# Kernel optimization log

Measured on AMD Instinct MI355X. Metric: run time of the kernel, lower is better.

The kernel has to match this reference:

```python
import jax, jax.numpy as jnp
import numpy as np

B = 256          # graph pairs
S = 128          # max_set_size (all graphs full-size)
D = 64           # node_state_dim (= filters_3)
DE = 32          # encoded edge dim
DM = 128         # message dim
DT = 32          # transform_dim
IN_N, IN_E = 16, 8
EPG = 1024       # edges per graph
NPROP = 5
SINK_ITERS = 20
TEMP = 0.1
N = 2 * B * S    # total nodes
E = 2 * B * EPG  # total edges


def setup_inputs() -> dict:
    key = jax.random.key(0)
    ks = jax.random.split(key, 32)
    def w(k, shp):
        return (jax.random.normal(k, shp, jnp.float32) / np.sqrt(shp[0])).astype(jnp.float32)
    base = jnp.repeat(jnp.arange(2 * B, dtype=jnp.int64) * S, EPG)
    from_idx = base + jax.random.randint(ks[0], (E,), 0, S).astype(jnp.int64)
    to_idx = base + jax.random.randint(ks[1], (E,), 0, S).astype(jnp.int64)
    return {
        'node_features': jax.random.normal(ks[2], (N, IN_N), jnp.float32),
        'edge_features': jax.random.normal(ks[3], (E, IN_E), jnp.float32),
        'W_enc_n': w(ks[4], (IN_N, D)),  'b_enc_n': jnp.zeros((D,), jnp.float32),
        'W_enc_e': w(ks[5], (IN_E, DE)), 'b_enc_e': jnp.zeros((DE,), jnp.float32),
        'W_c1': w(ks[6], (2 * D, 2 * D)), 'b_c1': jnp.zeros((2 * D,), jnp.float32),
        'W_c2': w(ks[7], (2 * D, D)),     'b_c2': jnp.zeros((D,), jnp.float32),
        'W_m1': w(ks[8], (2 * D + DE, DM)), 'b_m1': jnp.zeros((DM,), jnp.float32),
        'W_m2': w(ks[9], (DM, DM)),         'b_m2': jnp.zeros((DM,), jnp.float32),
        'W_u1': w(ks[10], (D + DM, DM)), 'b_u1': jnp.zeros((DM,), jnp.float32),
        'W_u2': w(ks[11], (DM, D)),      'b_u2': jnp.zeros((D,), jnp.float32),
        'W_t1': w(ks[12], (D, DT)), 'b_t1': jnp.zeros((DT,), jnp.float32),
        'W_t2': w(ks[13], (DT, DT)), 'b_t2': jnp.zeros((DT,), jnp.float32),
        'from_idx': from_idx, 'to_idx': to_idx,
    }


def _sinkhorn(sim):
    # log-space sinkhorn normalization, fixed iteration count
    log_a = sim / TEMP
    for _ in range(SINK_ITERS):
        log_a = log_a - jax.nn.logsumexp(log_a, axis=2, keepdims=True)
        log_a = log_a - jax.nn.logsumexp(log_a, axis=1, keepdims=True)
    return jnp.exp(log_a)


def reference(node_features, edge_features, W_enc_n, b_enc_n, W_enc_e, b_enc_e,
              W_c1, b_c1, W_c2, b_c2, W_m1, b_m1, W_m2, b_m2,
              W_u1, b_u1, W_u2, b_u2, W_t1, b_t1, W_t2, b_t2,
              from_idx, to_idx):
    h_enc = node_features @ W_enc_n + b_enc_n          # [N, D]
    e_enc = edge_features @ W_enc_e + b_enc_e          # [E, DE]

    def prop(h):
        # bidirectional messages, shared params (GMN GraphPropLayer, mlp update)
        hf, ht = h[from_idx], h[to_idx]
        m_f = jnp.concatenate([hf, ht, e_enc], -1)
        m_f = jax.nn.relu(m_f @ W_m1 + b_m1) @ W_m2 + b_m2
        m_r = jnp.concatenate([ht, hf, e_enc], -1)
        m_r = jax.nn.relu(m_r @ W_m1 + b_m1) @ W_m2 + b_m2
        agg = jax.ops.segment_sum(m_f, to_idx, num_segments=N) \
            + jax.ops.segment_sum(m_r, from_idx, num_segments=N)
        u = jnp.concatenate([h, agg], -1)
        return jax.nn.relu(u @ W_u1 + b_u1) @ W_u2 + b_u2

    h = h_enc
    store = jnp.zeros_like(h_enc)
    for _ in range(NPROP):
        comb = jnp.concatenate([h, store], -1)
        comb = jax.nn.relu(comb @ W_c1 + b_c1) @ W_c2 + b_c2
        h = prop(comb)                                  # [N, D]
        padded = h.reshape(2 * B, S, D)                 # full graphs -> pad is reshape
        q, c = padded[0::2], padded[1::2]               # [B, S, D] each
        tq = jax.nn.relu(q @ W_t1 + b_t1) @ W_t2 + b_t2
        tc = jax.nn.relu(c @ W_t1 + b_t1) @ W_t2 + b_t2
        # masks are all-ones since every graph has S nodes
        sim = jnp.einsum('bid,bjd->bij', tq, tc)        # [B, S, S]
        T = _sinkhorn(sim)
        q_from_c = jnp.einsum('bij,bjd->bid', T, c)
        c_from_q = jnp.einsum('bij,bid->bjd', T, q)
        # interleave q0,c0,q1,c1,... then gather by node_indices (= arange here)
        store = jnp.stack([q_from_c, c_from_q], axis=1).reshape(N, D)
    scores = -jnp.sum(jax.nn.relu(q - jnp.einsum('bij,bjd->bid', T, c)), axis=(1, 2))
    return scores
```

## Files before the change

kernel.cpp:

```cpp
#include <hip/hip_runtime.h>
#include <hip/hip_bf16.h>

#define NNODE  65536
#define NEDGE  524288
#define NGRAPH 512
#define EPG    1024
#define NPROP  5
#define SINKI  20

typedef __attribute__((ext_vector_type(4))) float f32x4;
typedef __attribute__((ext_vector_type(8))) _Float16 f16x8;

static __device__ __forceinline__ void split2(float v, _Float16& h, _Float16& l) {
    h = (_Float16)v;
    l = (_Float16)(v - (float)h);
}

static __device__ __forceinline__ unsigned packsplit(float v) {
    _Float16 h = (_Float16)v;
    _Float16 lo2 = (_Float16)(v - (float)h);
    union { _Float16 f; unsigned short s; } uh, ul;
    uh.f = h; ul.f = lo2;
    return (unsigned)uh.s | ((unsigned)ul.s << 16);
}

static __device__ __forceinline__ void unpack8(uint4 a, uint4 b, f16x8& h, f16x8& l) {
    union { unsigned u[4]; f16x8 v; } H, L;
    H.u[0] = (a.x & 0xffffu) | (a.y << 16);
    H.u[1] = (a.z & 0xffffu) | (a.w << 16);
    H.u[2] = (b.x & 0xffffu) | (b.y << 16);
    H.u[3] = (b.z & 0xffffu) | (b.w << 16);
    L.u[0] = (a.x >> 16) | (a.y & 0xffff0000u);
    L.u[1] = (a.z >> 16) | (a.w & 0xffff0000u);
    L.u[2] = (b.x >> 16) | (b.y & 0xffff0000u);
    L.u[3] = (b.z >> 16) | (b.w & 0xffff0000u);
    h = H.v; l = L.v;
}

template<int IN, int OUT>
__global__ void enc_kernel(const float* __restrict__ x, const float* __restrict__ W,
                           const float* __restrict__ b, float* __restrict__ y, int rows) {
    int idx = blockIdx.x * blockDim.x + threadIdx.x;
    if (idx >= rows * OUT) return;
    int r = idx / OUT, o = idx % OUT;
    const float* xr = x + (size_t)r * IN;
    float acc = b[o];
#pragma unroll
    for (int k = 0; k < IN; ++k) acc = fmaf(xr[k], W[k * OUT + o], acc);
    y[idx] = acc;
}

template<int IN, int OUT>
__global__ void enc_split_kernel(const float* __restrict__ x, const float* __restrict__ W,
                                 const float* __restrict__ b,
                                 _Float16* __restrict__ yh, _Float16* __restrict__ yl, int rows) {
    int idx = blockIdx.x * blockDim.x + threadIdx.x;
    if (idx >= rows * OUT) return;
    int r = idx / OUT, o = idx % OUT;
    const float* xr = x + (size_t)r * IN;
    float acc = b[o];
#pragma unroll
    for (int k = 0; k < IN; ++k) acc = fmaf(xr[k], W[k * OUT + o], acc);
    _Float16 h, l; split2(acc, h, l);
    yh[idx] = h; yl[idx] = l;
}

__global__ void splitT_kernel(const float* __restrict__ W, _Float16* __restrict__ Wh,
                              _Float16* __restrict__ Wl, int K, int C) {
    int idx = blockIdx.x * blockDim.x + threadIdx.x;
    if (idx >= K * C) return;
    int k = idx / C, cc = idx % C;
    _Float16 h, l; split2(W[idx], h, l);
    Wh[(size_t)cc * K + k] = h;
    Wl[(size_t)cc * K + k] = l;
}

template<int IN1, int IN2, int HID, int OUT>
__global__ __launch_bounds__(256) void mlp2_kernel(
    const float* __restrict__ x1, const float* __restrict__ x2,
    const float* __restrict__ W1, const float* __restrict__ b1,
    const float* __restrict__ W2, const float* __restrict__ b2,
    float* __restrict__ y) {
    constexpr int IN = IN1 + IN2;
    constexpr int TR = 32;
    __shared__ float xs[TR][IN];
    __shared__ float hs[TR][HID];
    const int t = threadIdx.x;
    const int row0 = blockIdx.x * TR;

    constexpr int INQ = IN / 4;
    for (int idx = t; idx < TR * INQ; idx += 256) {
        int r = idx / INQ, k0 = (idx % INQ) * 4;
        float4 v;
        if (IN2 == 0 || k0 < IN1) v = *(const float4*)(x1 + (size_t)(row0 + r) * IN1 + k0);
        else                      v = *(const float4*)(x2 + (size_t)(row0 + r) * IN2 + (k0 - IN1));
        *(float4*)&xs[r][k0] = v;
    }
    __syncthreads();

    constexpr int HQ = HID / 4;
    for (int idx = t; idx < TR * HQ; idx += 256) {
        int r = idx / HQ, j0 = (idx % HQ) * 4;
        float a0 = b1[j0], a1 = b1[j0+1], a2 = b1[j0+2], a3 = b1[j0+3];
        const float* wp = W1 + j0;
#pragma unroll 8
        for (int k = 0; k < IN; ++k) {
            float xv = xs[r][k];
            float4 w = *(const float4*)(wp + k * HID);
            a0 = fmaf(xv, w.x, a0); a1 = fmaf(xv, w.y, a1);
            a2 = fmaf(xv, w.z, a2); a3 = fmaf(xv, w.w, a3);
        }
        *(float4*)&hs[r][j0] = make_float4(fmaxf(a0, 0.f), fmaxf(a1, 0.f),
                                           fmaxf(a2, 0.f), fmaxf(a3, 0.f));
    }
    __syncthreads();

    constexpr int OQ = OUT / 4;
    for (int idx = t; idx < TR * OQ; idx += 256) {
        int r = idx / OQ, d0 = (idx % OQ) * 4;
        float a0 = b2[d0], a1 = b2[d0+1], a2 = b2[d0+2], a3 = b2[d0+3];
        const float* wp = W2 + d0;
#pragma unroll 8
        for (int k = 0; k < HID; ++k) {
            float hv = hs[r][k];
            float4 w = *(const float4*)(wp + k * OUT);
            a0 = fmaf(hv, w.x, a0); a1 = fmaf(hv, w.y, a1);
            a2 = fmaf(hv, w.z, a2); a3 = fmaf(hv, w.w, a3);
        }
        *(float4*)(y + (size_t)(row0 + r) * OUT + d0) = make_float4(a0, a1, a2, a3);
    }
}

__global__ __launch_bounds__(512, 2) void msg_kernel(
    const float* __restrict__ c,
    const _Float16* __restrict__ eh, const _Float16* __restrict__ el,
    const int* __restrict__ from_idx, const int* __restrict__ to_idx,
    const _Float16* __restrict__ W1h, const _Float16* __restrict__ W1l, const float* __restrict__ b1,
    const _Float16* __restrict__ W2h, const _Float16* __restrict__ W2l, const float* __restrict__ b2,
    float* __restrict__ agg) {
    __shared__ float ag[128][128];
    __shared__ _Float16 csh[128 * 64];
    __shared__ _Float16 csl[128 * 64];
    __shared__ unsigned Hp[64 * 128];
    __shared__ int ef[1024], et[1024];
    const int g = blockIdx.x, t = threadIdx.x;
    const int l = t & 63, wid = t >> 6;
    const int rg = wid >> 2, cg = wid & 3;
    const int lr = l & 15, lk = (l >> 4) * 8;
    const int ebase = g * EPG, nbase = g * 128;

    f16x8 b1h[5][2], b1l[5][2], b2h[4][2], b2l[4][2];
#pragma unroll
    for (int kf = 0; kf < 5; ++kf)
#pragma unroll
        for (int cf = 0; cf < 2; ++cf) {
            int col = cg * 32 + cf * 16 + lr;
            b1h[kf][cf] = *(const f16x8*)&W1h[(size_t)col * 160 + kf * 32 + lk];
            b1l[kf][cf] = *(const f16x8*)&W1l[(size_t)col * 160 + kf * 32 + lk];
        }
#pragma unroll
    for (int kf = 0; kf < 4; ++kf)
#pragma unroll
        for (int cf = 0; cf < 2; ++cf) {
            int col = cg * 32 + cf * 16 + lr;
            b2h[kf][cf] = *(const f16x8*)&W2h[(size_t)col * 128 + kf * 32 + lk];
            b2l[kf][cf] = *(const f16x8*)&W2l[(size_t)col * 128 + kf * 32 + lk];
        }
    const float b1v[2] = { b1[cg * 32 + lr], b1[cg * 32 + 16 + lr] };
    const float b2v[2] = { b2[cg * 32 + lr], b2[cg * 32 + 16 + lr] };

    for (int idx = t; idx < 4096; idx += 512)
        ((float4*)ag)[idx] = make_float4(0.f, 0.f, 0.f, 0.f);
    {
        const float* cblk = c + (size_t)nbase * 64;
        char* chB = (char*)csh; char* clB = (char*)csl;
        for (int idx = t; idx < 8192; idx += 512) {
            int row = idx >> 6, k = idx & 63;
            _Float16 h, lo2; split2(cblk[idx], h, lo2);
            int byte = ((row << 7) | (k << 1)) ^ ((row & 7) << 4);
            *(_Float16*)(chB + byte) = h;
            *(_Float16*)(clB + byte) = lo2;
        }
    }
    for (int idx = t; idx < 1024; idx += 512) {
        ef[idx] = from_idx[ebase + idx] - nbase;
        et[idx] = to_idx[ebase + idx] - nbase;
    }
    __syncthreads();

    char* chB = (char*)csh; char* clB = (char*)csl;

    for (int tile = 0; tile < 32; ++tile) {
        f32x4 acc[2][2];
#pragma unroll
        for (int rf = 0; rf < 2; ++rf) {
            const int rloc = rg * 32 + rf * 16 + lr;
            const int R = tile * 64 + rloc;
            const int e2 = R >> 1, dir = R & 1;
            const int fi = ef[e2], ti = et[e2];
            const int rA = dir ? ti : fi, rB = dir ? fi : ti;
            const int swA = (rA & 7) << 4, swB = (rB & 7) << 4;
            f16x8 ah[5], al[5];
            ah[0] = *(const f16x8*)(chB + (((rA << 7) | (lk << 1)) ^ swA));
            al[0] = *(const f16x8*)(clB + (((rA << 7) | (lk << 1)) ^ swA));
            ah[1] = *(const f16x8*)(chB + (((rA << 7) | ((32 + lk) << 1)) ^ swA));
            al[1] = *(const f16x8*)(clB + (((rA << 7) | ((32 + lk) << 1)) ^ swA));
            ah[2] = *(const f16x8*)(chB + (((rB << 7) | (lk << 1)) ^ swB));
            al[2] = *(const f16x8*)(clB + (((rB << 7) | (lk << 1)) ^ swB));
            ah[3] = *(const f16x8*)(chB + (((rB << 7) | ((32 + lk) << 1)) ^ swB));
            al[3] = *(const f16x8*)(clB + (((rB << 7) | ((32 + lk) << 1)) ^ swB));
            ah[4] = *(const f16x8*)&eh[(size_t)(ebase + e2) * 32 + lk];
            al[4] = *(const f16x8*)&el[(size_t)(ebase + e2) * 32 + lk];
            acc[rf][0] = (f32x4){b1v[0], b1v[0], b1v[0], b1v[0]};
            acc[rf][1] = (f32x4){b1v[1], b1v[1], b1v[1], b1v[1]};
#pragma unroll
            for (int kf = 0; kf < 5; ++kf)
#pragma unroll
                for (int cf = 0; cf < 2; ++cf) {
                    acc[rf][cf] = __builtin_amdgcn_mfma_f32_16x16x32_f16(ah[kf], b1h[kf][cf], acc[rf][cf], 0, 0, 0);
                    acc[rf][cf] = __builtin_amdgcn_mfma_f32_16x16x32_f16(al[kf], b1h[kf][cf], acc[rf][cf], 0, 0, 0);
                    acc[rf][cf] = __builtin_amdgcn_mfma_f32_16x16x32_f16(ah[kf], b1l[kf][cf], acc[rf][cf], 0, 0, 0);
                }
        }
        __syncthreads();
#pragma unroll
        for (int rf = 0; rf < 2; ++rf)
#pragma unroll
            for (int cf = 0; cf < 2; ++cf) {
                const int col = cg * 32 + cf * 16 + lr;
#pragma unroll
                for (int q = 0; q < 4; ++q) {
                    const int row = rg * 32 + rf * 16 + (l >> 4) * 4 + q;
                    Hp[(row * 128 + col) ^ ((row & 7) << 2)] = packsplit(fmaxf(acc[rf][cf][q], 0.f));
                }
            }
        __syncthreads();
#pragma unroll
        for (int rf = 0; rf < 2; ++rf) {
            const int row = rg * 32 + rf * 16 + lr;
            const int sw = (row & 7) << 2;
            f32x4 acc2[2];
            acc2[0] = (f32x4){b2v[0], b2v[0], b2v[0], b2v[0]};
            acc2[1] = (f32x4){b2v[1], b2v[1], b2v[1], b2v[1]};
#pragma unroll
            for (int kf = 0; kf < 4; ++kf) {
                const int c0 = kf * 32 + lk;
                uint4 pa = *(const uint4*)&Hp[(row * 128 + c0) ^ sw];
                uint4 pb = *(const uint4*)&Hp[(row * 128 + c0 + 4) ^ sw];
                f16x8 xh, xl; unpack8(pa, pb, xh, xl);
#pragma unroll
                for (int cf = 0; cf < 2; ++cf) {
                    acc2[cf] = __builtin_amdgcn_mfma_f32_16x16x32_f16(xh, b2h[kf][cf], acc2[cf], 0, 0, 0);
                    acc2[cf] = __builtin_amdgcn_mfma_f32_16x16x32_f16(xl, b2h[kf][cf], acc2[cf], 0, 0, 0);
                    acc2[cf] = __builtin_amdgcn_mfma_f32_16x16x32_f16(xh, b2l[kf][cf], acc2[cf], 0, 0, 0);
                }
            }
            const int r0 = rg * 32 + rf * 16 + ((l >> 4) << 2);
            const int e0 = (tile * 64 + r0) >> 1;
            int dst[4] = { et[e0], ef[e0], et[e0 + 1], ef[e0 + 1] };
#pragma unroll
            for (int q = 0; q < 4; ++q)
#pragma unroll
                for (int cf = 0; cf < 2; ++cf) {
                    const int colq = cg * 32 + cf * 16 + lr;
                    atomicAdd(&ag[dst[q]][colq ^ ((dst[q] & 7) << 2)], acc2[cf][q]);
                }
        }
    }
    __syncthreads();
    float* aout = agg + (size_t)g * 128 * 128;
    for (int idx = t; idx < 4096; idx += 512) {
        int row = idx >> 5, c4 = (idx & 31) << 2;
        ((float4*)aout)[idx] = *(const float4*)&ag[row][c4 ^ ((row & 7) << 2)];
    }
}

__global__ __launch_bounds__(512) void sink_kernel(
    const float* __restrict__ tbuf, const float* __restrict__ h,
    float* __restrict__ store, float* __restrict__ scores, int do_score) {
    __shared__ float la[128][128];
    __shared__ float ub[2 * 128 * 66];
    __shared__ float pm[512], ps[512];
    const int p = blockIdx.x, t = threadIdx.x;
    const int w = t >> 6, l = t & 63;

    const float* tq_src = tbuf + (size_t)(2 * p)     * 128 * 32;
    const float* tc_src = tbuf + (size_t)(2 * p + 1) * 128 * 32;
    for (int idx = t; idx < 4096; idx += 512) {
        int i = idx >> 5, k = idx & 31;
        ub[i * 33 + k]            = tq_src[idx];
        ub[128 * 33 + i * 33 + k] = tc_src[idx];
    }
    __syncthreads();

    for (int idx = t; idx < 16384; idx += 512) {
        int i = idx >> 7, j = idx & 127;
        float acc = 0.f;
#pragma unroll
        for (int k = 0; k < 32; ++k)
            acc = fmaf(ub[i * 33 + k], ub[128 * 33 + j * 33 + k], acc);
        la[i][j] = acc * 10.f;
    }
    __syncthreads();

    for (int iter = 0; iter < SINKI; ++iter) {
        for (int r = w; r < 128; r += 8) {
            float a0 = la[r][l], a1 = la[r][l + 64];
            float mx = fmaxf(a0, a1);
#pragma unroll
            for (int off = 32; off >= 1; off >>= 1) mx = fmaxf(mx, __shfl_xor(mx, off));
            float s = __expf(a0 - mx) + __expf(a1 - mx);
#pragma unroll
            for (int off = 32; off >= 1; off >>= 1) s += __shfl_xor(s, off);
            float lse = mx + __logf(s);
            la[r][l]      = a0 - lse;
            la[r][l + 64] = a1 - lse;
        }
        __syncthreads();
        const int j = t & 127, q4 = t >> 7, i0 = q4 * 32;
        float mx = -INFINITY;
        for (int i = i0; i < i0 + 32; ++i) mx = fmaxf(mx, la[i][j]);
        pm[t] = mx;
        __syncthreads();
        const float M = fmaxf(fmaxf(pm[j], pm[j + 128]), fmaxf(pm[j + 256], pm[j + 384]));
        float s = 0.f;
        for (int i = i0; i < i0 + 32; ++i) s += __expf(la[i][j] - M);
        ps[t] = s;
        __syncthreads();
        const float lse = M + __logf(ps[j] + ps[j + 128] + ps[j + 256] + ps[j + 384]);
        for (int i = i0; i < i0 + 32; ++i) la[i][j] -= lse;
        __syncthreads();
    }

    for (int idx = t; idx < 16384; idx += 512)
        ((float*)la)[idx] = __expf(((float*)la)[idx]);
    const float* hq_src = h + (size_t)(2 * p)     * 128 * 64;
    const float* hc_src = h + (size_t)(2 * p + 1) * 128 * 64;
    for (int idx = t; idx < 8192; idx += 512) {
        int i = idx >> 6, d = idx & 63;
        ub[i * 66 + d]            = hq_src[idx];
        ub[128 * 66 + i * 66 + d] = hc_src[idx];
    }
    __syncthreads();

    float sc = 0.f;
    float* store_q = store + (size_t)(2 * p)     * 128 * 64;
    float* store_c = store + (size_t)(2 * p + 1) * 128 * 64;
    for (int idx = t; idx < 8192; idx += 512) {
        int i = idx >> 6, d = idx & 63;
        float acc = 0.f;
#pragma unroll 8
        for (int j = 0; j < 128; ++j)
            acc = fmaf(la[i][j], ub[128 * 66 + j * 66 + d], acc);
        store_q[idx] = acc;
        if (do_score) sc += fmaxf(ub[i * 66 + d] - acc, 0.f);
    }
    for (int idx = t; idx < 8192; idx += 512) {
        int j = idx >> 6, d = idx & 63;
        float acc = 0.f;
#pragma unroll 8
        for (int i = 0; i < 128; ++i)
            acc = fmaf(la[i][j], ub[i * 66 + d], acc);
        store_c[idx] = acc;
    }
    if (do_score) {
#pragma unroll
        for (int off = 32; off >= 1; off >>= 1) sc += __shfl_xor(sc, off);
        if (l == 0) pm[w] = sc;
        __syncthreads();
        if (t == 0) {
            float s8 = 0.f;
#pragma unroll
            for (int i = 0; i < 8; ++i) s8 += pm[i];
            scores[p] = -s8;
        }
    }
}

extern "C" void kernel_launch(void* const* d_in, const int* in_sizes, int n_in,
                              void* d_out, int out_size, void* d_ws, size_t ws_size,
                              hipStream_t stream) {
    const float* node_features = (const float*)d_in[0];
    const float* edge_features = (const float*)d_in[1];
    const float* W_enc_n = (const float*)d_in[2];
    const float* b_enc_n = (const float*)d_in[3];
    const float* W_enc_e = (const float*)d_in[4];
    const float* b_enc_e = (const float*)d_in[5];
    const float* W_c1 = (const float*)d_in[6];
    const float* b_c1 = (const float*)d_in[7];
    const float* W_c2 = (const float*)d_in[8];
    const float* b_c2 = (const float*)d_in[9];
    const float* W_m1 = (const float*)d_in[10];
    const float* b_m1 = (const float*)d_in[11];
    const float* W_m2 = (const float*)d_in[12];
    const float* b_m2 = (const float*)d_in[13];
    const float* W_u1 = (const float*)d_in[14];
    const float* b_u1 = (const float*)d_in[15];
    const float* W_u2 = (const float*)d_in[16];
    const float* b_u2 = (const float*)d_in[17];
    const float* W_t1 = (const float*)d_in[18];
    const float* b_t1 = (const float*)d_in[19];
    const float* W_t2 = (const float*)d_in[20];
    const float* b_t2 = (const float*)d_in[21];
    const int* from_idx = (const int*)d_in[22];
    const int* to_idx   = (const int*)d_in[23];
    float* scores = (float*)d_out;

    char* ws = (char*)d_ws;
    size_t off = 0;
    auto alloc = [&](size_t bytes) { char* p = ws + off; off += (bytes + 255) & ~(size_t)255; return p; };
    float* h    = (float*)alloc((size_t)NNODE * 64 * 4);
    float* st   = (float*)alloc((size_t)NNODE * 64 * 4);
    float* cbuf = (float*)alloc((size_t)NNODE * 64 * 4);
    float* aggb = (float*)alloc((size_t)NNODE * 128 * 4);
    float* tb   = (float*)alloc((size_t)NNODE * 32 * 4);
    _Float16* eench = (_Float16*)alloc((size_t)NEDGE * 32 * 2);
    _Float16* eencl = (_Float16*)alloc((size_t)NEDGE * 32 * 2);
    _Float16* Wm1h = (_Float16*)alloc(160 * 128 * 2);
    _Float16* Wm1l = (_Float16*)alloc(160 * 128 * 2);
    _Float16* Wm2h = (_Float16*)alloc(128 * 128 * 2);
    _Float16* Wm2l = (_Float16*)alloc(128 * 128 * 2);
    (void)ws_size; (void)in_sizes; (void)n_in; (void)out_size;

    hipMemsetAsync(st, 0, (size_t)NNODE * 64 * sizeof(float), stream);
    enc_kernel<16, 64><<<(NNODE * 64 + 255) / 256, 256, 0, stream>>>(node_features, W_enc_n, b_enc_n, h, NNODE);
    enc_split_kernel<8, 32><<<(NEDGE * 32 + 255) / 256, 256, 0, stream>>>(edge_features, W_enc_e, b_enc_e, eench, eencl, NEDGE);
    splitT_kernel<<<(160 * 128 + 255) / 256, 256, 0, stream>>>(W_m1, Wm1h, Wm1l, 160, 128);
    splitT_kernel<<<(128 * 128 + 255) / 256, 256, 0, stream>>>(W_m2, Wm2h, Wm2l, 128, 128);

    for (int it = 0; it < NPROP; ++it) {
        mlp2_kernel<64, 64, 128, 64><<<NNODE / 32, 256, 0, stream>>>(h, st, W_c1, b_c1, W_c2, b_c2, cbuf);
        msg_kernel<<<NGRAPH, 512, 0, stream>>>(
            cbuf, eench, eencl, from_idx, to_idx, Wm1h, Wm1l, b_m1, Wm2h, Wm2l, b_m2, aggb);
        mlp2_kernel<64, 128, 128, 64><<<NNODE / 32, 256, 0, stream>>>(cbuf, aggb, W_u1, b_u1, W_u2, b_u2, h);
        mlp2_kernel<64, 0, 32, 32><<<NNODE / 32, 256, 0, stream>>>(h, nullptr, W_t1, b_t1, W_t2, b_t2, tb);
        sink_kernel<<<256, 512, 0, stream>>>(tb, h, st, scores, it == NPROP - 1 ? 1 : 0);
    }
}
```

Before: 8.210 ms.

## Widen message kernel to 1024 threads and fuse update and transform MLPs

The message kernel now runs 16 waves per graph, each wave owning one 16-column slice instead of two. Layer-2 weights are loaded from global memory inside the tile loop instead of being held in registers, which cuts register pressure and allows the larger block. Separately, the update MLP and the transform MLP are fused into one kernel that reuses the update output from shared memory, removing a launch and a reread of h. The risks are extra global/L2 weight traffic per tile and the single-block-per-CU launch bound limiting occupancy.

```diff
diff --git a/kernel.cpp b/kernel.cpp
--- a/kernel.cpp
+++ b/kernel.cpp
@@ -131,7 +131,97 @@
     }
 }
 
-__global__ __launch_bounds__(512, 2) void msg_kernel(
+__global__ __launch_bounds__(256) void ut_mlp_kernel(
+    const float* __restrict__ x1, const float* __restrict__ x2,
+    const float* __restrict__ W1, const float* __restrict__ b1,
+    const float* __restrict__ W2, const float* __restrict__ b2,
+    const float* __restrict__ Wt1, const float* __restrict__ bt1,
+    const float* __restrict__ Wt2, const float* __restrict__ bt2,
+    float* __restrict__ y, float* __restrict__ tb) {
+    constexpr int IN1 = 64, IN2 = 128, HID = 128, OUT = 64;
+    constexpr int IN = IN1 + IN2;
+    constexpr int TR = 32;
+    __shared__ float xs[TR][IN];
+    __shared__ float hs[TR][HID];
+    float (*ho)[OUT] = (float(*)[OUT])xs;
+    float (*th)[32]  = (float(*)[32])hs;
+    const int t = threadIdx.x;
+    const int row0 = blockIdx.x * TR;
+
+    constexpr int INQ = IN / 4;
+    for (int idx = t; idx < TR * INQ; idx += 256) {
+        int r = idx / INQ, k0 = (idx % INQ) * 4;
+        float4 v;
+        if (k0 < IN1) v = *(const float4*)(x1 + (size_t)(row0 + r) * IN1 + k0);
+        else          v = *(const float4*)(x2 + (size_t)(row0 + r) * IN2 + (k0 - IN1));
+        *(float4*)&xs[r][k0] = v;
+    }
+    __syncthreads();
+
+    constexpr int HQ = HID / 4;
+    for (int idx = t; idx < TR * HQ; idx += 256) {
+        int r = idx / HQ, j0 = (idx % HQ) * 4;
+        float a0 = b1[j0], a1 = b1[j0+1], a2 = b1[j0+2], a3 = b1[j0+3];
+        const float* wp = W1 + j0;
+#pragma unroll 8
+        for (int k = 0; k < IN; ++k) {
+            float xv = xs[r][k];
+            float4 w = *(const float4*)(wp + k * HID);
+            a0 = fmaf(xv, w.x, a0); a1 = fmaf(xv, w.y, a1);
+            a2 = fmaf(xv, w.z, a2); a3 = fmaf(xv, w.w, a3);
+        }
+        *(float4*)&hs[r][j0] = make_float4(fmaxf(a0, 0.f), fmaxf(a1, 0.f),
+                                           fmaxf(a2, 0.f), fmaxf(a3, 0.f));
+    }
+    __syncthreads();
+    constexpr int OQ = OUT / 4;
+    for (int idx = t; idx < TR * OQ; idx += 256) {
+        int r = idx / OQ, d0 = (idx % OQ) * 4;
+        float a0 = b2[d0], a1 = b2[d0+1], a2 = b2[d0+2], a3 = b2[d0+3];
+        const float* wp = W2 + d0;
+#pragma unroll 8
+        for (int k = 0; k < HID; ++k) {
+            float hv = hs[r][k];
+            float4 w = *(const float4*)(wp + k * OUT);
+            a0 = fmaf(hv, w.x, a0); a1 = fmaf(hv, w.y, a1);
+            a2 = fmaf(hv, w.z, a2); a3 = fmaf(hv, w.w, a3);
+        }
+        float4 v = make_float4(a0, a1, a2, a3);
+        *(float4*)(y + (size_t)(row0 + r) * OUT + d0) = v;
+        *(float4*)&ho[r][d0] = v;
+    }
+    __syncthreads();
+    for (int idx = t; idx < TR * 8; idx += 256) {
+        int r = idx >> 3, j0 = (idx & 7) * 4;
+        float a0 = bt1[j0], a1 = bt1[j0+1], a2 = bt1[j0+2], a3 = bt1[j0+3];
+        const float* wp = Wt1 + j0;
+#pragma unroll 8
+        for (int k = 0; k < 64; ++k) {
+            float xv = ho[r][k];
+            float4 w = *(const float4*)(wp + k * 32);
+            a0 = fmaf(xv, w.x, a0); a1 = fmaf(xv, w.y, a1);
+            a2 = fmaf(xv, w.z, a2); a3 = fmaf(xv, w.w, a3);
+        }
+        *(float4*)&th[r][j0] = make_float4(fmaxf(a0, 0.f), fmaxf(a1, 0.f),
+                                           fmaxf(a2, 0.f), fmaxf(a3, 0.f));
+    }
+    __syncthreads();
+    for (int idx = t; idx < TR * 8; idx += 256) {
+        int r = idx >> 3, o0 = (idx & 7) * 4;
+        float a0 = bt2[o0], a1 = bt2[o0+1], a2 = bt2[o0+2], a3 = bt2[o0+3];
+        const float* wp = Wt2 + o0;
+#pragma unroll
+        for (int k = 0; k < 32; ++k) {
+            float hv = th[r][k];
+            float4 w = *(const float4*)(wp + k * 32);
+            a0 = fmaf(hv, w.x, a0); a1 = fmaf(hv, w.y, a1);
+            a2 = fmaf(hv, w.z, a2); a3 = fmaf(hv, w.w, a3);
+        }
+        *(float4*)(tb + (size_t)(row0 + r) * 32 + o0) = make_float4(a0, a1, a2, a3);
+    }
+}
+
+__global__ __launch_bounds__(1024, 1) void msg_kernel(
     const float* __restrict__ c,
     const _Float16* __restrict__ eh, const _Float16* __restrict__ el,
     const int* __restrict__ from_idx, const int* __restrict__ to_idx,
@@ -145,36 +235,26 @@
     __shared__ int ef[1024], et[1024];
     const int g = blockIdx.x, t = threadIdx.x;
     const int l = t & 63, wid = t >> 6;
-    const int rg = wid >> 2, cg = wid & 3;
+    const int rg = wid >> 3, cg = wid & 7;
     const int lr = l & 15, lk = (l >> 4) * 8;
     const int ebase = g * EPG, nbase = g * 128;
-
-    f16x8 b1h[5][2], b1l[5][2], b2h[4][2], b2l[4][2];
-#pragma unroll
-    for (int kf = 0; kf < 5; ++kf)
-#pragma unroll
-        for (int cf = 0; cf < 2; ++cf) {
-            int col = cg * 32 + cf * 16 + lr;
-            b1h[kf][cf] = *(const f16x8*)&W1h[(size_t)col * 160 + kf * 32 + lk];
-            b1l[kf][cf] = *(const f16x8*)&W1l[(size_t)col * 160 + kf * 32 + lk];
-        }
-#pragma unroll
-    for (int kf = 0; kf < 4; ++kf)
-#pragma unroll
-        for (int cf = 0; cf < 2; ++cf) {
-            int col = cg * 32 + cf * 16 + lr;
-            b2h[kf][cf] = *(const f16x8*)&W2h[(size_t)col * 128 + kf * 32 + lk];
-            b2l[kf][cf] = *(const f16x8*)&W2l[(size_t)col * 128 + kf * 32 + lk];
-        }
-    const float b1v[2] = { b1[cg * 32 + lr], b1[cg * 32 + 16 + lr] };
-    const float b2v[2] = { b2[cg * 32 + lr], b2[cg * 32 + 16 + lr] };
-
-    for (int idx = t; idx < 4096; idx += 512)
+    const int col = cg * 16 + lr;
+
+    f16x8 b1h[5], b1l[5];
+#pragma unroll
+    for (int kf = 0; kf < 5; ++kf) {
+        b1h[kf] = *(const f16x8*)&W1h[(size_t)col * 160 + kf * 32 + lk];
+        b1l[kf] = *(const f16x8*)&W1l[(size_t)col * 160 + kf * 32 + lk];
+    }
+    const float b1v = b1[col];
+    const float b2v = b2[col];
+
+    for (int idx = t; idx < 4096; idx += 1024)
         ((float4*)ag)[idx] = make_float4(0.f, 0.f, 0.f, 0.f);
     {
         const float* cblk = c + (size_t)nbase * 64;
         char* chB = (char*)csh; char* clB = (char*)csl;
-        for (int idx = t; idx < 8192; idx += 512) {
+        for (int idx = t; idx < 8192; idx += 1024) {
             int row = idx >> 6, k = idx & 63;
             _Float16 h, lo2; split2(cblk[idx], h, lo2);
             int byte = ((row << 7) | (k << 1)) ^ ((row & 7) << 4);
@@ -182,7 +262,7 @@
             *(_Float16*)(clB + byte) = lo2;
         }
     }
-    for (int idx = t; idx < 1024; idx += 512) {
+    for (int idx = t; idx < 1024; idx += 1024) {
         ef[idx] = from_idx[ebase + idx] - nbase;
         et[idx] = to_idx[ebase + idx] - nbase;
     }
@@ -191,11 +271,10 @@
     char* chB = (char*)csh; char* clB = (char*)csl;
 
     for (int tile = 0; tile < 32; ++tile) {
-        f32x4 acc[2][2];
+        f32x4 acc[2];
 #pragma unroll
         for (int rf = 0; rf < 2; ++rf) {
-            const int rloc = rg * 32 + rf * 16 + lr;
-            const int R = tile * 64 + rloc;
+            const int R = tile * 64 + rg * 32 + rf * 16 + lr;
             const int e2 = R >> 1, dir = R & 1;
             const int fi = ef[e2], ti = et[e2];
             const int rA = dir ? ti : fi, rB = dir ? fi : ti;
@@ -211,65 +290,51 @@
             al[3] = *(const f16x8*)(clB + (((rB << 7) | ((32 + lk) << 1)) ^ swB));
             ah[4] = *(const f16x8*)&eh[(size_t)(ebase + e2) * 32 + lk];
             al[4] = *(const f16x8*)&el[(size_t)(ebase + e2) * 32 + lk];
-            acc[rf][0] = (f32x4){b1v[0], b1v[0], b1v[0], b1v[0]};
-            acc[rf][1] = (f32x4){b1v[1], b1v[1], b1v[1], b1v[1]};
-#pragma unroll
-            for (int kf = 0; kf < 5; ++kf)
-#pragma unroll
-                for (int cf = 0; cf < 2; ++cf) {
-                    acc[rf][cf] = __builtin_amdgcn_mfma_f32_16x16x32_f16(ah[kf], b1h[kf][cf], acc[rf][cf], 0, 0, 0);
-                    acc[rf][cf] = __builtin_amdgcn_mfma_f32_16x16x32_f16(al[kf], b1h[kf][cf], acc[rf][cf], 0, 0, 0);
-                    acc[rf][cf] = __builtin_amdgcn_mfma_f32_16x16x32_f16(ah[kf], b1l[kf][cf], acc[rf][cf], 0, 0, 0);
-                }
+            acc[rf] = (f32x4){b1v, b1v, b1v, b1v};
+#pragma unroll
+            for (int kf = 0; kf < 5; ++kf) {
+                acc[rf] = __builtin_amdgcn_mfma_f32_16x16x32_f16(ah[kf], b1h[kf], acc[rf], 0, 0, 0);
+                acc[rf] = __builtin_amdgcn_mfma_f32_16x16x32_f16(al[kf], b1h[kf], acc[rf], 0, 0, 0);
+                acc[rf] = __builtin_amdgcn_mfma_f32_16x16x32_f16(ah[kf], b1l[kf], acc[rf], 0, 0, 0);
+            }
         }
         __syncthreads();
 #pragma unroll
         for (int rf = 0; rf < 2; ++rf)
 #pragma unroll
-            for (int cf = 0; cf < 2; ++cf) {
-                const int col = cg * 32 + cf * 16 + lr;
-#pragma unroll
-                for (int q = 0; q < 4; ++q) {
-                    const int row = rg * 32 + rf * 16 + (l >> 4) * 4 + q;
-                    Hp[(row * 128 + col) ^ ((row & 7) << 2)] = packsplit(fmaxf(acc[rf][cf][q], 0.f));
-                }
+            for (int q = 0; q < 4; ++q) {
+                const int row = rg * 32 + rf * 16 + (l >> 4) * 4 + q;
+                Hp[(row * 128 + col) ^ ((row & 7) << 2)] = packsplit(fmaxf(acc[rf][q], 0.f));
             }
         __syncthreads();
 #pragma unroll
         for (int rf = 0; rf < 2; ++rf) {
             const int row = rg * 32 + rf * 16 + lr;
             const int sw = (row & 7) << 2;
-            f32x4 acc2[2];
-            acc2[0] = (f32x4){b2v[0], b2v[0], b2v[0], b2v[0]};
-            acc2[1] = (f32x4){b2v[1], b2v[1], b2v[1], b2v[1]};
+            f32x4 acc2 = (f32x4){b2v, b2v, b2v, b2v};
 #pragma unroll
             for (int kf = 0; kf < 4; ++kf) {
                 const int c0 = kf * 32 + lk;
                 uint4 pa = *(const uint4*)&Hp[(row * 128 + c0) ^ sw];
                 uint4 pb = *(const uint4*)&Hp[(row * 128 + c0 + 4) ^ sw];
                 f16x8 xh, xl; unpack8(pa, pb, xh, xl);
-#pragma unroll
-                for (int cf = 0; cf < 2; ++cf) {
-                    acc2[cf] = __builtin_amdgcn_mfma_f32_16x16x32_f16(xh, b2h[kf][cf], acc2[cf], 0, 0, 0);
-                    acc2[cf] = __builtin_amdgcn_mfma_f32_16x16x32_f16(xl, b2h[kf][cf], acc2[cf], 0, 0, 0);
-                    acc2[cf] = __builtin_amdgcn_mfma_f32_16x16x32_f16(xh, b2l[kf][cf], acc2[cf], 0, 0, 0);
-                }
+                f16x8 w2h = *(const f16x8*)&W2h[(size_t)col * 128 + kf * 32 + lk];
+                f16x8 w2l = *(const f16x8*)&W2l[(size_t)col * 128 + kf * 32 + lk];
+                acc2 = __builtin_amdgcn_mfma_f32_16x16x32_f16(xh, w2h, acc2, 0, 0, 0);
+                acc2 = __builtin_amdgcn_mfma_f32_16x16x32_f16(xl, w2h, acc2, 0, 0, 0);
+                acc2 = __builtin_amdgcn_mfma_f32_16x16x32_f16(xh, w2l, acc2, 0, 0, 0);
             }
             const int r0 = rg * 32 + rf * 16 + ((l >> 4) << 2);
             const int e0 = (tile * 64 + r0) >> 1;
             int dst[4] = { et[e0], ef[e0], et[e0 + 1], ef[e0 + 1] };
 #pragma unroll
             for (int q = 0; q < 4; ++q)
-#pragma unroll
-                for (int cf = 0; cf < 2; ++cf) {
-                    const int colq = cg * 32 + cf * 16 + lr;
-                    atomicAdd(&ag[dst[q]][colq ^ ((dst[q] & 7) << 2)], acc2[cf][q]);
-                }
+                atomicAdd(&ag[dst[q]][col ^ ((dst[q] & 7) << 2)], acc2[q]);
         }
     }
     __syncthreads();
     float* aout = agg + (size_t)g * 128 * 128;
-    for (int idx = t; idx < 4096; idx += 512) {
+    for (int idx = t; idx < 4096; idx += 1024) {
         int row = idx >> 5, c4 = (idx & 31) << 2;
         ((float4*)aout)[idx] = *(const float4*)&ag[row][c4 ^ ((row & 7) << 2)];
     }
@@ -430,10 +495,10 @@
 
     for (int it = 0; it < NPROP; ++it) {
         mlp2_kernel<64, 64, 128, 64><<<NNODE / 32, 256, 0, stream>>>(h, st, W_c1, b_c1, W_c2, b_c2, cbuf);
-        msg_kernel<<<NGRAPH, 512, 0, stream>>>(
+        msg_kernel<<<NGRAPH, 1024, 0, stream>>>(
             cbuf, eench, eencl, from_idx, to_idx, Wm1h, Wm1l, b_m1, Wm2h, Wm2l, b_m2, aggb);
-        mlp2_kernel<64, 128, 128, 64><<<NNODE / 32, 256, 0, stream>>>(cbuf, aggb, W_u1, b_u1, W_u2, b_u2, h);
-        mlp2_kernel<64, 0, 32, 32><<<NNODE / 32, 256, 0, stream>>>(h, nullptr, W_t1, b_t1, W_t2, b_t2, tb);
+        ut_mlp_kernel<<<NNODE / 32, 256, 0, stream>>>(
+            cbuf, aggb, W_u1, b_u1, W_u2, b_u2, W_t1, b_t1, W_t2, b_t2, h, tb);
         sink_kernel<<<256, 512, 0, stream>>>(tb, h, st, scores, it == NPROP - 1 ? 1 : 0);
     }
 }
```

After: 8.542 ms. 1.04x slower.
